# Performance work log

Measured on AMD Instinct MI355X. Metric: run time of the kernel, lower is better.

The kernel has to match this reference:

```python
import jax, jax.numpy as jnp
import numpy as np

EPS = 1e-5
NUM_LAYERS = 3


def _batchnorm(h, g, b):
    mean = h.mean(axis=0)
    var = h.var(axis=0)  # biased variance, matches torch BatchNorm training math
    return (h - mean) * jax.lax.rsqrt(var + EPS) * g + b


def setup_inputs() -> dict:
    key = jax.random.key(0)
    ks = jax.random.split(key, 8)
    N, E, D, H, OUT = 100000, 1600000, 128, 128, 64
    s = 0.08  # weight scale for numerical sanity
    return {
        "x": jax.random.normal(ks[0], (N, D), jnp.float32),
        "edge_index": jax.random.randint(ks[1], (2, E), 0, N, jnp.int64),
        "Wl": jax.random.normal(ks[2], (NUM_LAYERS, D, H), jnp.float32) * s,
        "bl": jnp.zeros((NUM_LAYERS, H), jnp.float32),
        "Wr": jax.random.normal(ks[3], (NUM_LAYERS, D, H), jnp.float32) * s,
        "gamma": jnp.ones((NUM_LAYERS, H), jnp.float32),
        "beta": jnp.zeros((NUM_LAYERS, H), jnp.float32),
        "W1": jax.random.normal(ks[4], (D + NUM_LAYERS * H, 2 * OUT), jnp.float32) * s,
        "b1": jnp.zeros((2 * OUT,), jnp.float32),
        "g1": jnp.ones((2 * OUT,), jnp.float32),
        "be1": jnp.zeros((2 * OUT,), jnp.float32),
        "W2": jax.random.normal(ks[5], (2 * OUT, OUT), jnp.float32) * s,
        "b2": jnp.zeros((OUT,), jnp.float32),
    }


def reference(x, edge_index, Wl, bl, Wr, gamma, beta, W1, b1, g1, be1, W2, b2):
    # GraphSAGE: stacked SAGEConv(mean aggr) + BatchNorm + ReLU, JK-concat, 2-layer MLP head.
    # Dropout is identity (eval mode).
    N = x.shape[0]
    src, dst = edge_index[0], edge_index[1]
    deg = jax.ops.segment_sum(jnp.ones((src.shape[0],), x.dtype), dst, num_segments=N)
    inv_deg = (1.0 / jnp.maximum(deg, 1.0))[:, None]  # [N,1]
    xs = [x]
    h = x
    for i in range(NUM_LAYERS):
        # mean-aggregate neighbor features, then linear (same math as PyG SAGEConv)
        agg = jax.ops.segment_sum(h[src], dst, num_segments=N) * inv_deg  # [N,D]
        h = agg @ Wl[i] + bl[i] + h @ Wr[i]
        h = _batchnorm(h, gamma[i], beta[i])
        h = jax.nn.relu(h)
        xs.append(h)
    z = jnp.concatenate(xs, axis=-1)  # [N, D + L*H]
    z = _batchnorm(z @ W1 + b1, g1, be1)
    z = jax.nn.leaky_relu(z, negative_slope=0.01)
    return z @ W2 + b2
```

## Files before the change

kernel.cpp:

```cpp
#include <hip/hip_runtime.h>
#include <hip/hip_bf16.h>

#define CDIV(a,b) (((a)+(b)-1)/(b))

typedef __attribute__((ext_vector_type(8))) short short8_t;
typedef __attribute__((ext_vector_type(4))) float f32x4;

__device__ __forceinline__ float b2f(ushort u){
    union { uint i; float f; } v; v.i = ((uint)u) << 16; return v.f;
}
__device__ __forceinline__ ushort f2b(float f){
    __hip_bfloat16 h = __float2bfloat16(f);
    return *reinterpret_cast<ushort*>(&h);
}

__global__ __launch_bounds__(256) void k_bcount(
    const int* __restrict__ dst, int E, int nbuck, int* __restrict__ bcnt)
{
    __shared__ int cnt[512];
    const int t = threadIdx.x;
    for (int i = t; i < nbuck; i += 256) cnt[i] = 0;
    __syncthreads();
    const int e0 = blockIdx.x * 4096;
    #pragma unroll
    for (int q = 0; q < 16; ++q){
        int idx = e0 + q*256 + t;
        if (idx < E) atomicAdd(&cnt[dst[idx] >> 8], 1);
    }
    __syncthreads();
    for (int i = t; i < nbuck; i += 256){
        int c = cnt[i];
        if (c) atomicAdd(&bcnt[i], c);
    }
}

__global__ void k_bscan(const int* __restrict__ bcnt, int nbuck, int E,
                        int* __restrict__ bbase, int* __restrict__ gcur)
{
    __shared__ int s[512];
    int t = threadIdx.x;
    int v = (t < nbuck) ? bcnt[t] : 0;
    s[t] = v;
    __syncthreads();
    for (int off = 1; off < 512; off <<= 1){
        int x = (t >= off) ? s[t-off] : 0;
        __syncthreads();
        s[t] += x;
        __syncthreads();
    }
    if (t < nbuck){ int e = s[t] - v; bbase[t] = e; gcur[t] = e; }
    if (t == 0) bbase[nbuck] = E;
}

__global__ __launch_bounds__(256) void k_bucketA(
    const int* __restrict__ src, const int* __restrict__ dst, int E,
    int nbuck, int* __restrict__ gcur, uint* __restrict__ ebuf)
{
    __shared__ int cnt[512];
    __shared__ int base[512];
    const int t  = threadIdx.x;
    const int e0 = blockIdx.x * 4096;
    for (int i = t; i < nbuck; i += 256) cnt[i] = 0;
    __syncthreads();
    uint pk[16]; int mb[16];
    #pragma unroll
    for (int q = 0; q < 16; ++q){
        int idx = e0 + q*256 + t;
        int b = -1; uint pkv = 0;
        if (idx < E){
            int s = src[idx], d = dst[idx];
            b = d >> 8;
            pkv = (uint)s | ((uint)(d & 255) << 24);
            atomicAdd(&cnt[b], 1);
        }
        mb[q] = b; pk[q] = pkv;
    }
    __syncthreads();
    for (int i = t; i < nbuck; i += 256){
        int c = cnt[i];
        base[i] = c ? atomicAdd(&gcur[i], c) : 0;
    }
    __syncthreads();
    for (int i = t; i < nbuck; i += 256) cnt[i] = 0;
    __syncthreads();
    #pragma unroll
    for (int q = 0; q < 16; ++q){
        if (mb[q] >= 0){
            int b   = mb[q];
            int pos = base[b] + atomicAdd(&cnt[b], 1);
            ebuf[pos] = pk[q];
        }
    }
}

__global__ __launch_bounds__(256) void k_build(
    const uint* __restrict__ ebuf, const int* __restrict__ bbase,
    int N, int E, int* __restrict__ row_ptr, float* __restrict__ inv_deg,
    int* __restrict__ col_idx)
{
    __shared__ int cnt[256];
    __shared__ int scn[256];
    const int b = blockIdx.x;
    const int t = threadIdx.x;
    const int n0 = b << 8;
    const int ebase = bbase[b], eend = bbase[b+1];

    cnt[t] = 0;
    __syncthreads();
    for (int j = ebase + t; j < eend; j += 256)
        atomicAdd(&cnt[ebuf[j] >> 24], 1);
    __syncthreads();

    int d = cnt[t];
    scn[t] = d;
    __syncthreads();
    for (int off = 1; off < 256; off <<= 1){
        int x = (t >= off) ? scn[t-off] : 0;
        __syncthreads();
        scn[t] += x;
        __syncthreads();
    }
    int excl = scn[t] - d;
    int node = n0 + t;
    if (node < N){
        row_ptr[node] = ebase + excl;
        inv_deg[node] = 1.0f / (float)(d > 1 ? d : 1);
    }
    if (b == 0 && t == 0) row_ptr[N] = E;

    cnt[t] = excl;
    __syncthreads();
    for (int j = ebase + t; j < eend; j += 256){
        uint e = ebuf[j];
        int p = atomicAdd(&cnt[e >> 24], 1);
        col_idx[ebase + p] = (int)(e & 0xFFFFFFu);
    }
}

__global__ void k_cvt_x(const float* __restrict__ in, ushort* __restrict__ out, int n4){
    int i = blockIdx.x*blockDim.x + threadIdx.x;
    if (i >= n4) return;
    float4 v = reinterpret_cast<const float4*>(in)[i];
    ushort4 o; o.x=f2b(v.x); o.y=f2b(v.y); o.z=f2b(v.z); o.w=f2b(v.w);
    reinterpret_cast<ushort4*>(out)[i] = o;
}

__global__ void k_cvt_w(const float* __restrict__ Wl, const float* __restrict__ Wr,
                        const float* __restrict__ W1, const float* __restrict__ W2,
                        ushort* __restrict__ WtL, ushort* __restrict__ WtR,
                        ushort* __restrict__ Wt1, ushort* __restrict__ Wt2)
{
    int i = blockIdx.x*blockDim.x + threadIdx.x;
    const int S = 16384;
    if (i < 3*S){
        int s = i / S, r = i - s*S;
        int k = r >> 7, c = r & 127;
        WtL[s*S + c*128 + k] = f2b(Wl[i]);
    } else if (i < 6*S){
        i -= 3*S;
        int s = i / S, r = i - s*S;
        int k = r >> 7, c = r & 127;
        WtR[s*S + c*128 + k] = f2b(Wr[i]);
    } else if (i < 10*S){
        i -= 6*S;
        int s = i / S, r = i - s*S;
        int k = r >> 7, c = r & 127;
        Wt1[s*S + c*128 + k] = f2b(W1[i]);
    } else {
        i -= 10*S;
        if (i < 8192){
            int k = i >> 6, c = i & 63;
            Wt2[c*128 + k] = f2b(W2[i]);
        }
    }
}

template<int NORM>
__global__ __launch_bounds__(256) void k_agg_bf(
    const ushort* __restrict__ h, const int* __restrict__ row_ptr,
    const int* __restrict__ col_idx, const float* __restrict__ inv_deg,
    const float* __restrict__ ssp, ushort* __restrict__ agg, int N)
{
    int node = (blockIdx.x*blockDim.x + threadIdx.x) >> 6;
    int lane = threadIdx.x & 63;
    if (node >= N) return;
    const int g = lane >> 4, l15 = lane & 15;
    const int beg = row_ptr[node], end = row_ptr[node+1];
    const size_t co = (size_t)l15 * 8;

    float scv[8], shv[8];
    if (NORM){
        float4 c0 = *reinterpret_cast<const float4*>(ssp + co);
        float4 c1 = *reinterpret_cast<const float4*>(ssp + co + 4);
        float4 s0 = *reinterpret_cast<const float4*>(ssp + 128 + co);
        float4 s1 = *reinterpret_cast<const float4*>(ssp + 128 + co + 4);
        scv[0]=c0.x; scv[1]=c0.y; scv[2]=c0.z; scv[3]=c0.w;
        scv[4]=c1.x; scv[5]=c1.y; scv[6]=c1.z; scv[7]=c1.w;
        shv[0]=s0.x; shv[1]=s0.y; shv[2]=s0.z; shv[3]=s0.w;
        shv[4]=s1.x; shv[5]=s1.y; shv[6]=s1.z; shv[7]=s1.w;
    }

    float2 a2[4];
    #pragma unroll
    for (int q = 0; q < 4; ++q) a2[q] = make_float2(0.f, 0.f);

    auto acc8 = [&](uint4 v){
        uint w[4] = {v.x, v.y, v.z, v.w};
        #pragma unroll
        for (int q = 0; q < 4; ++q){
            union { uint i; float f; } lo, hi;
            lo.i = w[q] << 16;
            hi.i = w[q] & 0xffff0000u;
            float fl = lo.f, fh = hi.f;
            if (NORM){
                fl = fmaxf(fl*scv[2*q]   + shv[2*q],   0.f);
                fh = fmaxf(fh*scv[2*q+1] + shv[2*q+1], 0.f);
            }
            a2[q].x += fl;
            a2[q].y += fh;
        }
    };

    int j = beg + g;
    while (j + 4 < end){
        int s0 = col_idx[j];
        int s1 = col_idx[j+4];
        uint4 v0 = *reinterpret_cast<const uint4*>(h + (size_t)s0*128 + co);
        uint4 v1 = *reinterpret_cast<const uint4*>(h + (size_t)s1*128 + co);
        acc8(v0); acc8(v1);
        j += 8;
    }
    if (j < end){
        int s0 = col_idx[j];
        uint4 v0 = *reinterpret_cast<const uint4*>(h + (size_t)s0*128 + co);
        acc8(v0);
    }

    #pragma unroll
    for (int q = 0; q < 4; ++q){
        a2[q].x += __shfl_xor(a2[q].x, 16);
        a2[q].y += __shfl_xor(a2[q].y, 16);
        a2[q].x += __shfl_xor(a2[q].x, 32);
        a2[q].y += __shfl_xor(a2[q].y, 32);
    }

    if (g == 0){
        float sc = inv_deg[node];
        uint r[4];
        #pragma unroll
        for (int q = 0; q < 4; ++q)
            r[q] = (uint)f2b(a2[q].x*sc) | ((uint)f2b(a2[q].y*sc) << 16);
        *reinterpret_cast<uint4*>(agg + (size_t)node*128 + co) =
            make_uint4(r[0], r[1], r[2], r[3]);
    }
}

__device__ __forceinline__ short8_t norm_frag(short8_t a, const float* __restrict__ sp,
                                              int kbase, int leaky)
{
    float4 c0 = *reinterpret_cast<const float4*>(sp + kbase);
    float4 c1 = *reinterpret_cast<const float4*>(sp + kbase + 4);
    float4 h0 = *reinterpret_cast<const float4*>(sp + 128 + kbase);
    float4 h1 = *reinterpret_cast<const float4*>(sp + 128 + kbase + 4);
    float cs[8] = {c0.x,c0.y,c0.z,c0.w,c1.x,c1.y,c1.z,c1.w};
    float hs[8] = {h0.x,h0.y,h0.z,h0.w,h1.x,h1.y,h1.z,h1.w};
    uint* au = reinterpret_cast<uint*>(&a);
    short8_t r;
    uint* ru = reinterpret_cast<uint*>(&r);
    #pragma unroll
    for (int q = 0; q < 4; ++q){
        float lo = b2f((ushort)(au[q] & 0xffffu));
        float hi = b2f((ushort)(au[q] >> 16));
        lo = lo*cs[2*q]   + hs[2*q];
        hi = hi*cs[2*q+1] + hs[2*q+1];
        if (leaky){ lo = lo > 0.f ? lo : 0.01f*lo; hi = hi > 0.f ? hi : 0.01f*hi; }
        else      { lo = fmaxf(lo, 0.f); hi = fmaxf(hi, 0.f); }
        ru[q] = (uint)f2b(lo) | ((uint)f2b(hi) << 16);
    }
    return r;
}

template<int NCF, int STATS, int OUTBF>
__global__ __launch_bounds__(256) void k_gemm_mfma(
    const ushort* __restrict__ A0, const ushort* __restrict__ T0,
    const ushort* __restrict__ A1, const ushort* __restrict__ T1,
    const ushort* __restrict__ A2, const ushort* __restrict__ T2,
    const ushort* __restrict__ A3, const ushort* __restrict__ T3,
    const float* __restrict__ ns0, const float* __restrict__ ns1,
    const float* __restrict__ ns2, const float* __restrict__ ns3,
    int m0, int m1, int m2, int m3,
    int P, const float* __restrict__ bias,
    ushort* __restrict__ out_bf, float* __restrict__ out_f32,
    float* __restrict__ partials, int N)
{
    __shared__ ushort Ws[17920];
    const int t   = threadIdx.x;
    const int w   = t >> 6, l = t & 63;
    const int l15 = l & 15, lg = l >> 4;
    const int r0   = blockIdx.x * 128;
    const int wrow = w * 32;

    f32x4 acc[2][NCF];
    #pragma unroll
    for (int i = 0; i < 2; ++i)
        #pragma unroll
        for (int j = 0; j < NCF; ++j) acc[i][j] = (f32x4){0.f,0.f,0.f,0.f};

    for (int p = 0; p < P; ++p){
        const ushort* A  = (p==0)?A0:(p==1)?A1:(p==2)?A2:A3;
        const ushort* T  = (p==0)?T0:(p==1)?T1:(p==2)?T2:T3;
        const float*  ns = (p==0)?ns0:(p==1)?ns1:(p==2)?ns2:ns3;
        const int     md = (p==0)?m0:(p==1)?m1:(p==2)?m2:m3;
        if (p) __syncthreads();
        #pragma unroll
        for (int q = 0; q < NCF; ++q){
            int lin  = q*256 + t;
            int row  = lin >> 4, c16 = lin & 15;
            int c16s = c16 ^ (row & 7);
            uint4 v = *reinterpret_cast<const uint4*>(T + (size_t)row*128 + c16*8);
            *reinterpret_cast<uint4*>(&Ws[row*128 + c16s*8]) = v;
        }
        __syncthreads();
        #pragma unroll
        for (int kk = 0; kk < 4; ++kk){
            const int k0 = kk*32;
            short8_t a[2];
            #pragma unroll
            for (int rf = 0; rf < 2; ++rf){
                size_t gr = (size_t)(r0 + wrow + rf*16 + l15);
                a[rf] = *reinterpret_cast<const short8_t*>(A + gr*128 + k0 + lg*8);
            }
            if (md){
                a[0] = norm_frag(a[0], ns, k0 + lg*8, md == 2);
                a[1] = norm_frag(a[1], ns, k0 + lg*8, md == 2);
            }
            #pragma unroll
            for (int cf = 0; cf < NCF; ++cf){
                int row  = cf*16 + l15;
                int c16  = (k0 >> 3) + lg;
                int c16s = c16 ^ (row & 7);
                short8_t b = *reinterpret_cast<const short8_t*>(&Ws[row*128 + c16s*8]);
                acc[0][cf] = __builtin_amdgcn_mfma_f32_16x16x32_bf16(a[0], b, acc[0][cf], 0, 0, 0);
                acc[1][cf] = __builtin_amdgcn_mfma_f32_16x16x32_bf16(a[1], b, acc[1][cf], 0, 0, 0);
            }
        }
    }

    float bs[NCF];
    #pragma unroll
    for (int cf = 0; cf < NCF; ++cf) bs[cf] = bias[cf*16 + l15];

    float s1[NCF], s2[NCF];
    #pragma unroll
    for (int cf = 0; cf < NCF; ++cf){ s1[cf] = 0.f; s2[cf] = 0.f; }

    __syncthreads();

    #pragma unroll
    for (int rf = 0; rf < 2; ++rf){
        #pragma unroll
        for (int q = 0; q < 4; ++q){
            int row_l = wrow + rf*16 + lg*4 + q;
            bool valid = (r0 + row_l) < N;
            #pragma unroll
            for (int cf = 0; cf < NCF; ++cf){
                float v = acc[rf][cf][q] + bs[cf];
                if (STATS && valid){ s1[cf] += v; s2[cf] += v*v; }
                if (OUTBF) Ws[row_l*140 + cf*16 + l15] = f2b(v);
                else       reinterpret_cast<float*>(Ws)[row_l*70 + cf*16 + l15] = v;
            }
        }
    }
    __syncthreads();

    const int tr = t >> 4, tc = t & 15;
    #pragma unroll
    for (int i = 0; i < 8; ++i){
        int row_l = i*16 + tr;
        int gr = r0 + row_l;
        if (gr < N){
            if (OUTBF){
                uint4 v = *reinterpret_cast<const uint4*>(&Ws[row_l*140 + tc*8]);
                *reinterpret_cast<uint4*>(&out_bf[(size_t)gr*(NCF*16) + tc*8]) = v;
            } else {
                float4 v = *reinterpret_cast<const float4*>(
                    &reinterpret_cast<float*>(Ws)[row_l*70 + tc*4]);
                *reinterpret_cast<float4*>(&out_f32[(size_t)gr*(NCF*16) + tc*4]) = v;
            }
        }
    }

    if (STATS){
        #pragma unroll
        for (int cf = 0; cf < NCF; ++cf){
            s1[cf] += __shfl_xor(s1[cf], 16);
            s1[cf] += __shfl_xor(s1[cf], 32);
            s2[cf] += __shfl_xor(s2[cf], 16);
            s2[cf] += __shfl_xor(s2[cf], 32);
        }
        if (l < 16){
            float* pb = partials + (size_t)(blockIdx.x*4 + w)*256;
            #pragma unroll
            for (int cf = 0; cf < NCF; ++cf){
                pb[cf*16 + l15]       = s1[cf];
                pb[128 + cf*16 + l15] = s2[cf];
            }
        }
    }
}

__global__ void k_bnreduce(const float* __restrict__ partials, int I, int N,
                           const float* __restrict__ gamma, const float* __restrict__ beta,
                           float* __restrict__ ss)
{
    int c = blockIdx.x;
    int l = threadIdx.x;
    float s1 = 0.f, s2 = 0.f;
    for (int i = l; i < I; i += 64){
        s1 += partials[(size_t)i*256 + c];
        s2 += partials[(size_t)i*256 + 128 + c];
    }
    #pragma unroll
    for (int off = 32; off; off >>= 1){
        s1 += __shfl_xor(s1, off);
        s2 += __shfl_xor(s2, off);
    }
    if (l == 0){
        float m   = s1 / (float)N;
        float var = s2 / (float)N - m*m;
        float sc  = rsqrtf(var + 1e-5f) * gamma[c];
        ss[c]     = sc;
        ss[128+c] = beta[c] - m*sc;
    }
}

extern "C" void kernel_launch(void* const* d_in, const int* in_sizes, int n_in,
                              void* d_out, int out_size, void* d_ws, size_t ws_size,
                              hipStream_t stream)
{
    const float* x     = (const float*)d_in[0];
    const int*   ei    = (const int*)  d_in[1];
    const float* Wl    = (const float*)d_in[2];
    const float* bl    = (const float*)d_in[3];
    const float* Wr    = (const float*)d_in[4];
    const float* gamma = (const float*)d_in[5];
    const float* beta  = (const float*)d_in[6];
    const float* W1    = (const float*)d_in[7];
    const float* b1    = (const float*)d_in[8];
    const float* g1    = (const float*)d_in[9];
    const float* be1   = (const float*)d_in[10];
    const float* W2    = (const float*)d_in[11];
    const float* b2    = (const float*)d_in[12];
    float* out = (float*)d_out;

    const int N  = in_sizes[0] / 128;
    const int E  = in_sizes[1] / 2;
    const int NB = CDIV(N, 128);
    const size_t NPAD = (size_t)NB * 128;
    const int* src = ei;
    const int* dst = ei + E;

    const int NBUCK = CDIV(N, 256);

    char* w = (char*)d_ws;
    const size_t SB = NPAD * 128 * sizeof(ushort);
    ushort* x_bf = (ushort*)(w + 0*SB);
    ushort* pre0 = (ushort*)(w + 1*SB);
    ushort* pre1 = (ushort*)(w + 2*SB);
    ushort* pre2 = (ushort*)(w + 3*SB);
    ushort* aggb = (ushort*)(w + 4*SB);
    ushort* preh = (ushort*)(w + 5*SB);
    char* p = w + 6*SB;
    ushort* WtL = (ushort*)p;  p += (size_t)3*16384*2;
    ushort* WtR = (ushort*)p;  p += (size_t)3*16384*2;
    ushort* Wt1 = (ushort*)p;  p += (size_t)4*16384*2;
    ushort* Wt2 = (ushort*)p;  p += (size_t)8192*2;
    float* partials = (float*)p; p += (size_t)NB*4*256*sizeof(float);
    uint*  ebuf     = (uint*)p;  p += (size_t)E*4;
    int*   col_idx  = (int*)p;   p += (size_t)E*4;
    int*   row_ptr  = (int*)p;   p += (size_t)(N+1)*4;
    float* inv_deg  = (float*)p; p += (size_t)N*4;
    int*   bcnt     = (int*)p;   p += 512*4;
    int*   bbase    = (int*)p;   p += 516*4;
    int*   gcur     = (int*)p;   p += 512*4;
    float* ss0      = (float*)p; p += 256*4;
    float* ss1      = (float*)p; p += 256*4;
    float* ss2      = (float*)p; p += 256*4;
    float* ssh      = (float*)p; p += 256*4;

    const int n4 = N * 32;
    k_cvt_x<<<CDIV(n4,256), 256, 0, stream>>>(x, x_bf, n4);
    k_cvt_w<<<CDIV(10*16384+8192,256), 256, 0, stream>>>(Wl, Wr, W1, W2, WtL, WtR, Wt1, Wt2);

    hipMemsetAsync(bcnt, 0, 512*4, stream);
    k_bcount<<<CDIV(E,4096), 256, 0, stream>>>(dst, E, NBUCK, bcnt);
    k_bscan<<<1, 512, 0, stream>>>(bcnt, NBUCK, E, bbase, gcur);
    k_bucketA<<<CDIV(E,4096), 256, 0, stream>>>(src, dst, E, NBUCK, gcur, ebuf);
    k_build<<<NBUCK, 256, 0, stream>>>(ebuf, bbase, N, E, row_ptr, inv_deg, col_idx);

    ushort* pre[3] = {pre0, pre1, pre2};
    float*  ssl[3] = {ss0, ss1, ss2};
    const int I = NB * 4;

    for (int L = 0; L < 3; ++L){
        if (L == 0)
            k_agg_bf<0><<<CDIV(N,4), 256, 0, stream>>>(x_bf, row_ptr, col_idx, inv_deg,
                                                       nullptr, aggb, N);
        else
            k_agg_bf<1><<<CDIV(N,4), 256, 0, stream>>>(pre[L-1], row_ptr, col_idx, inv_deg,
                                                       ssl[L-1], aggb, N);
        const ushort* hsrc = (L == 0) ? x_bf : pre[L-1];
        const float*  hns  = (L == 0) ? nullptr : ssl[L-1];
        int hmode = (L == 0) ? 0 : 1;
        k_gemm_mfma<8,1,1><<<NB, 256, 0, stream>>>(
            aggb, WtL + (size_t)L*16384,
            hsrc, WtR + (size_t)L*16384,
            nullptr, nullptr, nullptr, nullptr,
            nullptr, hns, nullptr, nullptr,
            0, hmode, 0, 0,
            2, bl + (size_t)L*128, pre[L], nullptr, partials, N);
        k_bnreduce<<<128, 64, 0, stream>>>(partials, I, N,
            gamma + (size_t)L*128, beta + (size_t)L*128, ssl[L]);
    }

    k_gemm_mfma<8,1,1><<<NB, 256, 0, stream>>>(
        x_bf, Wt1 + 0,
        pre0, Wt1 + 16384,
        pre1, Wt1 + 2*16384,
        pre2, Wt1 + 3*16384,
        nullptr, ss0, ss1, ss2,
        0, 1, 1, 1,
        4, b1, preh, nullptr, partials, N);
    k_bnreduce<<<128, 64, 0, stream>>>(partials, I, N, g1, be1, ssh);

    k_gemm_mfma<4,0,0><<<NB, 256, 0, stream>>>(
        preh, Wt2, nullptr, nullptr, nullptr, nullptr, nullptr, nullptr,
        ssh, nullptr, nullptr, nullptr,
        2, 0, 0, 0,
        1, b2, nullptr, out, partials, N);
}
```

Before: 481.1 us.

## Degree-sort nodes and split aggregation into four column slices per node

Adds a counting sort of nodes by in-degree (histogram, scan, scatter) to produce a processing order. The aggregation kernel now gives each node four threads per 32-column slice, with four grid slices covering the 128 features, walking edges serially without cross-lane shuffles. Degree-sorted order is meant to balance work across a wavefront and cut divergence. The BN partial reduction also moves from 64 to 256 threads per channel. The costs are three extra preprocessing kernels, narrower 64-byte gathers per edge spread over four slices, and less edge-level parallelism for high-degree nodes.

Result: slower. 687.7 us (+42.9%).

```diff
diff --git a/kernel.cpp b/kernel.cpp
--- a/kernel.cpp
+++ b/kernel.cpp
@@ -134,6 +134,69 @@
         uint e = ebuf[j];
         int p = atomicAdd(&cnt[e >> 24], 1);
         col_idx[ebase + p] = (int)(e & 0xFFFFFFu);
+    }
+}
+
+__global__ __launch_bounds__(256) void k_dhist(
+    const int* __restrict__ row_ptr, int N, int* __restrict__ hist)
+{
+    __shared__ int h[512];
+    int t = threadIdx.x;
+    for (int i = t; i < 512; i += 256) h[i] = 0;
+    __syncthreads();
+    for (int n = blockIdx.x*256 + t; n < N; n += gridDim.x*256){
+        int d = min(row_ptr[n+1] - row_ptr[n], 511);
+        atomicAdd(&h[d], 1);
+    }
+    __syncthreads();
+    for (int i = t; i < 512; i += 256){
+        int v = h[i];
+        if (v) atomicAdd(&hist[i], v);
+    }
+}
+
+__global__ void k_dscan(const int* __restrict__ hist, int* __restrict__ dcur)
+{
+    __shared__ int s[512];
+    int t = threadIdx.x;
+    int v = hist[t];
+    s[t] = v;
+    __syncthreads();
+    for (int off = 1; off < 512; off <<= 1){
+        int x = (t >= off) ? s[t-off] : 0;
+        __syncthreads();
+        s[t] += x;
+        __syncthreads();
+    }
+    dcur[t] = s[t] - v;
+}
+
+__global__ __launch_bounds__(256) void k_dscatter(
+    const int* __restrict__ row_ptr, int N, int* __restrict__ dcur,
+    int* __restrict__ order)
+{
+    __shared__ int cnt[512];
+    __shared__ int base[512];
+    int t = threadIdx.x;
+    for (int i = t; i < 512; i += 256) cnt[i] = 0;
+    __syncthreads();
+    int n = blockIdx.x*256 + t;
+    int d = -1;
+    if (n < N){
+        d = min(row_ptr[n+1] - row_ptr[n], 511);
+        atomicAdd(&cnt[d], 1);
+    }
+    __syncthreads();
+    for (int i = t; i < 512; i += 256){
+        int c = cnt[i];
+        base[i] = c ? atomicAdd(&dcur[i], c) : 0;
+    }
+    __syncthreads();
+    for (int i = t; i < 512; i += 256) cnt[i] = 0;
+    __syncthreads();
+    if (n < N){
+        int p = base[d] + atomicAdd(&cnt[d], 1);
+        order[p] = n;
     }
 }
 
@@ -176,17 +239,24 @@
 }
 
 template<int NORM>
-__global__ __launch_bounds__(256) void k_agg_bf(
+__global__ __launch_bounds__(256) void k_agg4(
     const ushort* __restrict__ h, const int* __restrict__ row_ptr,
     const int* __restrict__ col_idx, const float* __restrict__ inv_deg,
-    const float* __restrict__ ssp, ushort* __restrict__ agg, int N)
-{
-    int node = (blockIdx.x*blockDim.x + threadIdx.x) >> 6;
-    int lane = threadIdx.x & 63;
-    if (node >= N) return;
-    const int g = lane >> 4, l15 = lane & 15;
+    const int* __restrict__ order, const float* __restrict__ ssp,
+    ushort* __restrict__ agg, int N)
+{
+    const int slice = blockIdx.x & 3;
+    const int slot  = (blockIdx.x >> 2)*64 + (threadIdx.x >> 2);
+    if (slot >= N) return;
+    const int l4   = threadIdx.x & 3;
+    const int node = order[slot];
     const int beg = row_ptr[node], end = row_ptr[node+1];
-    const size_t co = (size_t)l15 * 8;
+    const uint co = (uint)slice*32u + (uint)l4*8u;
+    const ushort* hs = h + co;
+
+    float a[8];
+    #pragma unroll
+    for (int q = 0; q < 8; ++q) a[q] = 0.f;
 
     float scv[8], shv[8];
     if (NORM){
@@ -200,11 +270,7 @@
         shv[4]=s1.x; shv[5]=s1.y; shv[6]=s1.z; shv[7]=s1.w;
     }
 
-    float2 a2[4];
-    #pragma unroll
-    for (int q = 0; q < 4; ++q) a2[q] = make_float2(0.f, 0.f);
-
-    auto acc8 = [&](uint4 v){
+    auto accv = [&](uint4 v){
         uint w[4] = {v.x, v.y, v.z, v.w};
         #pragma unroll
         for (int q = 0; q < 4; ++q){
@@ -216,43 +282,31 @@
                 fl = fmaxf(fl*scv[2*q]   + shv[2*q],   0.f);
                 fh = fmaxf(fh*scv[2*q+1] + shv[2*q+1], 0.f);
             }
-            a2[q].x += fl;
-            a2[q].y += fh;
+            a[2*q]   += fl;
+            a[2*q+1] += fh;
         }
     };
 
-    int j = beg + g;
-    while (j + 4 < end){
-        int s0 = col_idx[j];
-        int s1 = col_idx[j+4];
-        uint4 v0 = *reinterpret_cast<const uint4*>(h + (size_t)s0*128 + co);
-        uint4 v1 = *reinterpret_cast<const uint4*>(h + (size_t)s1*128 + co);
-        acc8(v0); acc8(v1);
-        j += 8;
+    int j = beg;
+    for (; j + 1 < end; j += 2){
+        uint s0 = (uint)col_idx[j];
+        uint s1 = (uint)col_idx[j+1];
+        uint4 v0 = *reinterpret_cast<const uint4*>(hs + (size_t)s0*128u);
+        uint4 v1 = *reinterpret_cast<const uint4*>(hs + (size_t)s1*128u);
+        accv(v0); accv(v1);
     }
     if (j < end){
-        int s0 = col_idx[j];
-        uint4 v0 = *reinterpret_cast<const uint4*>(h + (size_t)s0*128 + co);
-        acc8(v0);
-    }
-
-    #pragma unroll
-    for (int q = 0; q < 4; ++q){
-        a2[q].x += __shfl_xor(a2[q].x, 16);
-        a2[q].y += __shfl_xor(a2[q].y, 16);
-        a2[q].x += __shfl_xor(a2[q].x, 32);
-        a2[q].y += __shfl_xor(a2[q].y, 32);
-    }
-
-    if (g == 0){
-        float sc = inv_deg[node];
-        uint r[4];
-        #pragma unroll
-        for (int q = 0; q < 4; ++q)
-            r[q] = (uint)f2b(a2[q].x*sc) | ((uint)f2b(a2[q].y*sc) << 16);
-        *reinterpret_cast<uint4*>(agg + (size_t)node*128 + co) =
-            make_uint4(r[0], r[1], r[2], r[3]);
-    }
+        uint s0 = (uint)col_idx[j];
+        accv(*reinterpret_cast<const uint4*>(hs + (size_t)s0*128u));
+    }
+
+    float sc = inv_deg[node];
+    uint r[4];
+    #pragma unroll
+    for (int q = 0; q < 4; ++q)
+        r[q] = (uint)f2b(a[2*q]*sc) | ((uint)f2b(a[2*q+1]*sc) << 16);
+    *reinterpret_cast<uint4*>(agg + (size_t)node*128u + co) =
+        make_uint4(r[0], r[1], r[2], r[3]);
 }
 
 __device__ __forceinline__ short8_t norm_frag(short8_t a, const float* __restrict__ sp,
@@ -409,25 +463,28 @@
     }
 }
 
-__global__ void k_bnreduce(const float* __restrict__ partials, int I, int N,
-                           const float* __restrict__ gamma, const float* __restrict__ beta,
-                           float* __restrict__ ss)
-{
+__global__ __launch_bounds__(256) void k_bnreduce(
+    const float* __restrict__ partials, int I, int N,
+    const float* __restrict__ gamma, const float* __restrict__ beta,
+    float* __restrict__ ss)
+{
+    __shared__ float red[512];
     int c = blockIdx.x;
-    int l = threadIdx.x;
+    int t = threadIdx.x;
     float s1 = 0.f, s2 = 0.f;
-    for (int i = l; i < I; i += 64){
+    for (int i = t; i < I; i += 256){
         s1 += partials[(size_t)i*256 + c];
         s2 += partials[(size_t)i*256 + 128 + c];
     }
-    #pragma unroll
-    for (int off = 32; off; off >>= 1){
-        s1 += __shfl_xor(s1, off);
-        s2 += __shfl_xor(s2, off);
-    }
-    if (l == 0){
-        float m   = s1 / (float)N;
-        float var = s2 / (float)N - m*m;
+    red[t] = s1; red[256+t] = s2;
+    __syncthreads();
+    for (int off = 128; off; off >>= 1){
+        if (t < off){ red[t] += red[t+off]; red[256+t] += red[256+t+off]; }
+        __syncthreads();
+    }
+    if (t == 0){
+        float m   = red[0] / (float)N;
+        float var = red[256] / (float)N - m*m;
         float sc  = rsqrtf(var + 1e-5f) * gamma[c];
         ss[c]     = sc;
         ss[128+c] = beta[c] - m*sc;
@@ -480,9 +537,12 @@
     int*   col_idx  = (int*)p;   p += (size_t)E*4;
     int*   row_ptr  = (int*)p;   p += (size_t)(N+1)*4;
     float* inv_deg  = (float*)p; p += (size_t)N*4;
+    int*   order    = (int*)p;   p += (size_t)N*4;
     int*   bcnt     = (int*)p;   p += 512*4;
     int*   bbase    = (int*)p;   p += 516*4;
     int*   gcur     = (int*)p;   p += 512*4;
+    int*   dhist    = (int*)p;   p += 512*4;
+    int*   dcur     = (int*)p;   p += 512*4;
     float* ss0      = (float*)p; p += 256*4;
     float* ss1      = (float*)p; p += 256*4;
     float* ss2      = (float*)p; p += 256*4;
@@ -493,22 +553,28 @@
     k_cvt_w<<<CDIV(10*16384+8192,256), 256, 0, stream>>>(Wl, Wr, W1, W2, WtL, WtR, Wt1, Wt2);
 
     hipMemsetAsync(bcnt, 0, 512*4, stream);
+    hipMemsetAsync(dhist, 0, 512*4, stream);
     k_bcount<<<CDIV(E,4096), 256, 0, stream>>>(dst, E, NBUCK, bcnt);
     k_bscan<<<1, 512, 0, stream>>>(bcnt, NBUCK, E, bbase, gcur);
     k_bucketA<<<CDIV(E,4096), 256, 0, stream>>>(src, dst, E, NBUCK, gcur, ebuf);
     k_build<<<NBUCK, 256, 0, stream>>>(ebuf, bbase, N, E, row_ptr, inv_deg, col_idx);
 
+    k_dhist<<<256, 256, 0, stream>>>(row_ptr, N, dhist);
+    k_dscan<<<1, 512, 0, stream>>>(dhist, dcur);
+    k_dscatter<<<CDIV(N,256), 256, 0, stream>>>(row_ptr, N, dcur, order);
+
     ushort* pre[3] = {pre0, pre1, pre2};
     float*  ssl[3] = {ss0, ss1, ss2};
     const int I = NB * 4;
+    const int AGG_GRID = CDIV(N,64) * 4;
 
     for (int L = 0; L < 3; ++L){
         if (L == 0)
-            k_agg_bf<0><<<CDIV(N,4), 256, 0, stream>>>(x_bf, row_ptr, col_idx, inv_deg,
-                                                       nullptr, aggb, N);
+            k_agg4<0><<<AGG_GRID, 256, 0, stream>>>(x_bf, row_ptr, col_idx, inv_deg,
+                                                    order, nullptr, aggb, N);
         else
-            k_agg_bf<1><<<CDIV(N,4), 256, 0, stream>>>(pre[L-1], row_ptr, col_idx, inv_deg,
-                                                       ssl[L-1], aggb, N);
+            k_agg4<1><<<AGG_GRID, 256, 0, stream>>>(pre[L-1], row_ptr, col_idx, inv_deg,
+                                                    order, ssl[L-1], aggb, N);
         const ushort* hsrc = (L == 0) ? x_bf : pre[L-1];
         const float*  hns  = (L == 0) ? nullptr : ssl[L-1];
         int hmode = (L == 0) ? 0 : 1;
@@ -519,7 +585,7 @@
             nullptr, hns, nullptr, nullptr,
             0, hmode, 0, 0,
             2, bl + (size_t)L*128, pre[L], nullptr, partials, N);
-        k_bnreduce<<<128, 64, 0, stream>>>(partials, I, N,
+        k_bnreduce<<<128, 256, 0, stream>>>(partials, I, N,
             gamma + (size_t)L*128, beta + (size_t)L*128, ssl[L]);
     }
 
@@ -531,7 +597,7 @@
         nullptr, ss0, ss1, ss2,
         0, 1, 1, 1,
         4, b1, preh, nullptr, partials, N);
-    k_bnreduce<<<128, 64, 0, stream>>>(partials, I, N, g1, be1, ssh);
+    k_bnreduce<<<128, 256, 0, stream>>>(partials, I, N, g1, be1, ssh);
 
     k_gemm_mfma<4,0,0><<<NB, 256, 0, stream>>>(
         preh, Wt2, nullptr, nullptr, nullptr, nullptr, nullptr, nullptr,
```
